# Performance work log

Measured on AMD Instinct MI355X. Metric: run time of the kernel, lower is better.

The kernel has to match this reference:

```python
import jax, jax.numpy as jnp
import numpy as np

N_HEADS = 8
D_EMBED = 512
D_HEAD = D_EMBED // N_HEADS


def setup_inputs() -> dict:
    key = jax.random.key(0)
    ks = jax.random.split(key, 5)
    B, S, D = 8, 2048, D_EMBED
    scale_in = 1.0 / np.sqrt(D)
    x = jax.random.normal(ks[0], (B, S, D), dtype=jnp.float32)
    # torch nn.Linear weights: (out_features, in_features)
    w_in = jax.random.normal(ks[1], (3 * D, D), dtype=jnp.float32) * scale_in
    b_in = jax.random.normal(ks[2], (3 * D,), dtype=jnp.float32) * scale_in
    w_out = jax.random.normal(ks[3], (D, D), dtype=jnp.float32) * scale_in
    b_out = jax.random.normal(ks[4], (D,), dtype=jnp.float32) * scale_in
    return {"x": x, "w_in": w_in, "b_in": b_in, "w_out": w_out, "b_out": b_out}


def reference(x, w_in, b_in, w_out, b_out):
    B, S, D = x.shape
    H, Dh = N_HEADS, D_HEAD
    # fused QKV projection (torch Linear: x @ W^T + b)
    qkv = x @ w_in.T + b_in                     # (B, S, 3D)
    q, k, v = jnp.split(qkv, 3, axis=-1)        # each (B, S, D)
    # split heads -> (B, H, S, Dh)
    def heads(t):
        return t.reshape(B, S, H, Dh).transpose(0, 2, 1, 3)
    q, k, v = heads(q), heads(k), heads(v)
    # scaled dot-product attention (full matrix, as in source)
    scores = jnp.einsum("bhqd,bhkd->bhqk", q, k) / jnp.sqrt(jnp.float32(Dh))
    weights = jax.nn.softmax(scores, axis=-1)   # (B, H, S, S)
    out = jnp.einsum("bhqk,bhkd->bhqd", weights, v)
    out = out.transpose(0, 2, 1, 3).reshape(B, S, D)
    return out @ w_out.T + b_out
```

## Files before the change

### kernel.cpp

```cpp
#include <hip/hip_runtime.h>
#include <stdint.h>

#define SEQ   2048
#define DEMB  512
#define NH    8
#define DH    64
#define BATCH 8
#define M_ROWS (BATCH * SEQ)
#define QKLD  1024
#define QSCALE 0.18033688011112042f

typedef __attribute__((ext_vector_type(8))) __bf16 bf16x8;
typedef __attribute__((ext_vector_type(4))) __bf16 bf16x4;
typedef __attribute__((ext_vector_type(4))) float  f32x4;
typedef __attribute__((ext_vector_type(8))) uint16_t u16x8;
typedef __attribute__((ext_vector_type(4))) uint32_t u32x4;

__device__ __forceinline__ void gll16(const __bf16* g, __bf16* l) {
    __builtin_amdgcn_global_load_lds(
        (__attribute__((address_space(1))) void*)(__bf16*)g,
        (__attribute__((address_space(3))) void*)l, 16, 0, 0);
}

__device__ __forceinline__ bf16x8 ld8(const __bf16* p) {
    return *(const bf16x8*)p;
}

__device__ __forceinline__ uint32_t pkpair(float a, float b) {
    const uint16_t lo = __builtin_bit_cast(uint16_t, (__bf16)a);
    const uint16_t hi = __builtin_bit_cast(uint16_t, (__bf16)b);
    return (uint32_t)lo | ((uint32_t)hi << 16);
}

__device__ __forceinline__ int sw(int row, int chunk) {
    return row * 64 + ((chunk ^ (row & 7)) << 3);
}

__device__ __forceinline__ void stage_gll_sw(const __bf16* g, int gld,
                                             __bf16* l, int wave, int lane) {
    const int lr = lane >> 3;
    const int scol = ((lane & 7) ^ lr) * 8;
    #pragma unroll
    for (int i = 0; i < 2; i++) {
        const int r0 = i * 32 + wave * 8;
        gll16(g + (size_t)(r0 + lr) * gld + scol, l + r0 * 64);
    }
}

__device__ __forceinline__ void stage_gll(const __bf16* src, __bf16* dst,
                                          int ld, int wave, int lane) {
    const int srow = lane >> 3, scol = ((lane & 7) ^ srow) * 8;
    #pragma unroll
    for (int i = 0; i < 4; i++) {
        const int r0 = (i * 4 + wave) * 8;
        gll16(src + (size_t)(r0 + srow) * ld + scol, dst + r0 * 64);
    }
}

#define NXQ (M_ROWS * DEMB / 4)
#define NWQ (3 * DEMB * DEMB / 4)
#define NOQ (DEMB * DEMB / 4)

__global__ __launch_bounds__(256)
void cvt_all(const float* __restrict__ x, const float* __restrict__ w_in,
             __bf16* __restrict__ xb, __bf16* __restrict__ wb) {
    const int i = blockIdx.x * 256 + threadIdx.x;
    const float4* src;
    bf16x4* dst;
    if (i < NXQ) { src = (const float4*)x + i;         dst = (bf16x4*)xb + i; }
    else if (i < NXQ + NWQ) {
        const int j = i - NXQ;
        src = (const float4*)w_in + j;  dst = (bf16x4*)wb + j;
    } else return;
    const float4 v = *src;
    bf16x4 b;
    b[0] = (__bf16)v.x; b[1] = (__bf16)v.y;
    b[2] = (__bf16)v.z; b[3] = (__bf16)v.w;
    *dst = b;
}

__global__ __launch_bounds__(256)
void cvt_wout(const float* __restrict__ w, __bf16* __restrict__ wb) {
    const int i = blockIdx.x * 256 + threadIdx.x;
    if (i < NOQ) {
        const float4 v = ((const float4*)w)[i];
        bf16x4 b;
        b[0] = (__bf16)v.x; b[1] = (__bf16)v.y;
        b[2] = (__bf16)v.z; b[3] = (__bf16)v.w;
        ((bf16x4*)wb)[i] = b;
    }
}

__global__ __launch_bounds__(256)
void gemm_qkv(const __bf16* __restrict__ A, const __bf16* __restrict__ W,
              const float* __restrict__ bias, __bf16* __restrict__ qk,
              __bf16* __restrict__ vt) {
    constexpr int K = DEMB;
    __shared__ __align__(16) __bf16 SM[128 * 128];
    __bf16* As = SM;
    __bf16* Bs = SM + 128 * 64;

    const int tid  = threadIdx.x;
    const int wave = tid >> 6, lane = tid & 63;
    const int quad = lane >> 4, l16 = lane & 15;
    const int m0 = blockIdx.x * 128, n0 = blockIdx.y * 128;
    const int wm = wave & 1, wn = wave >> 1;
    const bool qkblk = (n0 < QKLD);

    f32x4 acc[4][4] = {};

    for (int k0 = 0; k0 < K; k0 += 64) {
        __syncthreads();
        stage_gll(A + (size_t)m0 * K + k0, As, K, wave, lane);
        stage_gll(W + (size_t)n0 * K + k0, Bs, K, wave, lane);
        __syncthreads();
        #pragma unroll
        for (int ks = 0; ks < 2; ks++) {
            bf16x8 af[4], bf[4];
            #pragma unroll
            for (int t = 0; t < 4; t++) {
                af[t] = ld8(&As[sw(wm * 64 + t * 16 + l16, ks * 4 + quad)]);
                bf[t] = ld8(&Bs[sw(wn * 64 + t * 16 + l16, ks * 4 + quad)]);
            }
            if (qkblk) {
                #pragma unroll
                for (int j = 0; j < 4; j++)
                    #pragma unroll
                    for (int i = 0; i < 4; i++)
                        acc[j][i] = __builtin_amdgcn_mfma_f32_16x16x32_bf16(
                            bf[j], af[i], acc[j][i], 0, 0, 0);
            } else {
                #pragma unroll
                for (int i = 0; i < 4; i++)
                    #pragma unroll
                    for (int j = 0; j < 4; j++)
                        acc[i][j] = __builtin_amdgcn_mfma_f32_16x16x32_bf16(
                            af[i], bf[j], acc[i][j], 0, 0, 0);
            }
        }
    }

    __syncthreads();

    if (qkblk) {
        const float scl = (n0 < DEMB) ? QSCALE : 1.0f;
        #pragma unroll
        for (int j = 0; j < 4; j++) {
            const int nl = wn * 64 + j * 16 + quad * 4;
            const float4 bv4 = *(const float4*)&bias[n0 + nl];
            const int chunk = nl >> 3;
            #pragma unroll
            for (int i = 0; i < 4; i++) {
                const int ml = wm * 64 + i * 16 + l16;
                bf16x4 pk;
                pk[0] = (__bf16)((acc[j][i][0] + bv4.x) * scl);
                pk[1] = (__bf16)((acc[j][i][1] + bv4.y) * scl);
                pk[2] = (__bf16)((acc[j][i][2] + bv4.z) * scl);
                pk[3] = (__bf16)((acc[j][i][3] + bv4.w) * scl);
                const int phys = ((chunk & 7) ^ (ml & 7)) | (chunk & 8);
                *(bf16x4*)(&SM[ml * 128 + phys * 8 + (nl & 7)]) = pk;
            }
        }
        __syncthreads();
        const int g = tid >> 4, li = tid & 15;
        #pragma unroll
        for (int it = 0; it < 8; it++) {
            const int row = it * 16 + g;
            const int phys = ((li & 7) ^ (row & 7)) | (li & 8);
            bf16x8 v = ld8(&SM[row * 128 + phys * 8]);
            *(bf16x8*)(qk + (size_t)(m0 + row) * QKLD + n0 + li * 8) = v;
        }
    } else {
        const int hd0 = n0 - QKLD;
        const int bb = m0 >> 11, s0 = m0 & (SEQ - 1);
        #pragma unroll
        for (int j = 0; j < 4; j++) {
            const int n = n0 + wn * 64 + j * 16 + l16;
            const float bv = bias[n];
            const int hdl = wn * 64 + j * 16 + l16;
            #pragma unroll
            for (int i = 0; i < 4; i++) {
                const int sl = wm * 64 + i * 16 + quad * 4;
                bf16x4 pk;
                #pragma unroll
                for (int r = 0; r < 4; r++)
                    pk[r] = (__bf16)(acc[i][j][r] + bv);
                const int chunk = sl >> 3;
                const int phys = (((chunk & 7) ^ (hdl & 7)) | (chunk & 8));
                *(bf16x4*)(&SM[hdl * 128 + phys * 8 + (sl & 7)]) = pk;
            }
        }
        __syncthreads();
        const int g = tid >> 4, li = tid & 15;
        #pragma unroll
        for (int it = 0; it < 8; it++) {
            const int row = it * 16 + g;
            const int phys = (((li & 7) ^ (row & 7)) | (li & 8));
            bf16x8 v = ld8(&SM[row * 128 + phys * 8]);
            *(bf16x8*)(vt + ((size_t)(bb * DEMB + hd0 + row)) * SEQ + s0 + li * 8) = v;
        }
    }
}

__global__ __launch_bounds__(256, 4)
void attn_flash(const __bf16* __restrict__ qk, const __bf16* __restrict__ vt,
                __bf16* __restrict__ outp) {
    const int qt = blockIdx.x, h = blockIdx.y, b = blockIdx.z;
    const int tid  = threadIdx.x;
    const int wave = tid >> 6, lane = tid & 63;
    const int quad = lane >> 4, l16 = lane & 15;

    __shared__ __align__(16) __bf16 Ks[2][64 * 64];
    __shared__ __align__(16) __bf16 Vt[2][64 * 64];

    const size_t brow = (size_t)b * SEQ;
    const int q0 = qt * 128 + wave * 32;
    const __bf16* kbase = qk + brow * QKLD + DEMB + h * DH;
    const __bf16* vbase = vt + ((size_t)(b * DEMB + h * DH)) * SEQ;

    const u16x8 one16 = {0x3F80, 0x3F80, 0x3F80, 0x3F80,
                         0x3F80, 0x3F80, 0x3F80, 0x3F80};
    const bf16x8 ONES = __builtin_bit_cast(bf16x8, one16);

    bf16x8 qf[2][2];
    #pragma unroll
    for (int qb = 0; qb < 2; qb++) {
        const __bf16* qp = qk + (brow + q0 + qb * 16 + l16) * QKLD + h * DH + quad * 8;
        qf[qb][0] = ld8(qp);
        qf[qb][1] = ld8(qp + 32);
    }

    f32x4 o[2][4] = {};
    f32x4 osum[2] = {};
    uint32_t pk[2][4][2];
    bf16x8 pf[2][2];

    auto do_qkexp = [&](int tt) {
        const int bufq = tt & 1;
        #pragma unroll
        for (int kt = 0; kt < 4; kt++) {
            bf16x8 kf0 = ld8(&Ks[bufq][sw(kt * 16 + l16, quad)]);
            bf16x8 kf1 = ld8(&Ks[bufq][sw(kt * 16 + l16, 4 + quad)]);
            #pragma unroll
            for (int qb = 0; qb < 2; qb++) {
                f32x4 c = {};
                c = __builtin_amdgcn_mfma_f32_16x16x32_bf16(kf0, qf[qb][0], c, 0, 0, 0);
                c = __builtin_amdgcn_mfma_f32_16x16x32_bf16(kf1, qf[qb][1], c, 0, 0, 0);
                pk[qb][kt][0] = pkpair(__builtin_amdgcn_exp2f(c[0]),
                                       __builtin_amdgcn_exp2f(c[1]));
                pk[qb][kt][1] = pkpair(__builtin_amdgcn_exp2f(c[2]),
                                       __builtin_amdgcn_exp2f(c[3]));
            }
        }
    };

    auto do_permlane_osum = [&]() {
        #pragma unroll
        for (int qb = 0; qb < 2; qb++) {
            #pragma unroll
            for (int f = 0; f < 2; f++) {
                uint32_t a0 = pk[qb][2 * f][0], b0 = pk[qb][2 * f + 1][0];
                uint32_t a1 = pk[qb][2 * f][1], b1 = pk[qb][2 * f + 1][1];
                {
                    auto r = __builtin_amdgcn_permlane32_swap(a0, b0, false, false);
                    a0 = r[0]; b0 = r[1];
                }
                {
                    auto r = __builtin_amdgcn_permlane32_swap(a1, b1, false, false);
                    a1 = r[0]; b1 = r[1];
                }
                {
                    auto r = __builtin_amdgcn_permlane16_swap(a0, b0, false, false);
                    a0 = r[0]; b0 = r[1];
                }
                {
                    auto r = __builtin_amdgcn_permlane16_swap(a1, b1, false, false);
                    a1 = r[0]; b1 = r[1];
                }
                u32x4 d;
                d[0] = a0; d[1] = a1; d[2] = b0; d[3] = b1;
                pf[qb][f] = __builtin_bit_cast(bf16x8, d);
            }
            osum[qb] = __builtin_amdgcn_mfma_f32_16x16x32_bf16(pf[qb][0], ONES, osum[qb], 0, 0, 0);
            osum[qb] = __builtin_amdgcn_mfma_f32_16x16x32_bf16(pf[qb][1], ONES, osum[qb], 0, 0, 0);
        }
    };

    auto do_pv = [&](int tt) {
        const int bufv = tt & 1;
        #pragma unroll
        for (int db = 0; db < 4; db++) {
            bf16x8 vf0 = ld8(&Vt[bufv][sw(db * 16 + l16, quad)]);
            bf16x8 vf1 = ld8(&Vt[bufv][sw(db * 16 + l16, 4 + quad)]);
            #pragma unroll
            for (int qb = 0; qb < 2; qb++) {
                o[qb][db] = __builtin_amdgcn_mfma_f32_16x16x32_bf16(pf[qb][0], vf0, o[qb][db], 0, 0, 0);
                o[qb][db] = __builtin_amdgcn_mfma_f32_16x16x32_bf16(pf[qb][1], vf1, o[qb][db], 0, 0, 0);
            }
        }
    };

    constexpr int NT = SEQ / 64;

    stage_gll_sw(kbase,                      QKLD, Ks[0], wave, lane);
    stage_gll_sw(vbase,                      SEQ,  Vt[0], wave, lane);
    stage_gll_sw(kbase + (size_t)64 * QKLD,  QKLD, Ks[1], wave, lane);
    __syncthreads();
    do_qkexp(0);

    for (int t = 0; t < NT - 1; ++t) {
        __syncthreads();
        if (t + 2 < NT)
            stage_gll_sw(kbase + (size_t)(t + 2) * 64 * QKLD, QKLD, Ks[t & 1], wave, lane);
        stage_gll_sw(vbase + (t + 1) * 64, SEQ, Vt[(t + 1) & 1], wave, lane);

        do_permlane_osum();
        __builtin_amdgcn_s_setprio(1);
        do_pv(t);
        do_qkexp(t + 1);
        __builtin_amdgcn_s_setprio(0);
    }

    __syncthreads();
    do_permlane_osum();
    do_pv(NT - 1);

    #pragma unroll
    for (int qb = 0; qb < 2; qb++)
        #pragma unroll
        for (int r = 0; r < 4; r++) {
            const float linv = __builtin_amdgcn_rcpf(osum[qb][r]);
            const int q = q0 + qb * 16 + quad * 4 + r;
            #pragma unroll
            for (int db = 0; db < 4; db++)
                outp[(brow + q) * DEMB + h * DH + db * 16 + l16] =
                    (__bf16)(o[qb][db][r] * linv);
        }
}

__global__ __launch_bounds__(256)
void gemm_out(const __bf16* __restrict__ A, const __bf16* __restrict__ W,
              const float* __restrict__ bias, float* __restrict__ C,
              int N, int K) {
    __shared__ __align__(16) __bf16 SMO[2 * 128 * 64];
    __bf16* As = SMO;
    __bf16* Bs = SMO + 128 * 64;

    const int tid  = threadIdx.x;
    const int wave = tid >> 6, lane = tid & 63;
    const int quad = lane >> 4, l16 = lane & 15;
    const int m0 = blockIdx.x * 128, n0 = blockIdx.y * 128;
    const int wm = wave & 1, wn = wave >> 1;

    f32x4 acc[4][4] = {};

    for (int k0 = 0; k0 < K; k0 += 64) {
        __syncthreads();
        stage_gll(A + (size_t)m0 * K + k0, As, K, wave, lane);
        stage_gll(W + (size_t)n0 * K + k0, Bs, K, wave, lane);
        __syncthreads();
        #pragma unroll
        for (int ks = 0; ks < 2; ks++) {
            bf16x8 af[4], bf[4];
            #pragma unroll
            for (int t = 0; t < 4; t++) {
                af[t] = ld8(&As[sw(wm * 64 + t * 16 + l16, ks * 4 + quad)]);
                bf[t] = ld8(&Bs[sw(wn * 64 + t * 16 + l16, ks * 4 + quad)]);
            }
            #pragma unroll
            for (int j = 0; j < 4; j++)
                #pragma unroll
                for (int i = 0; i < 4; i++)
                    acc[j][i] = __builtin_amdgcn_mfma_f32_16x16x32_bf16(
                        bf[j], af[i], acc[j][i], 0, 0, 0);
        }
    }

    __syncthreads();
    float* SMf = (float*)SMO;

    #pragma unroll
    for (int p = 0; p < 2; p++) {
        if (p) __syncthreads();
        if (wm == p) {
            #pragma unroll
            for (int j = 0; j < 4; j++) {
                const int nl = wn * 64 + j * 16 + quad * 4;
                const float4 bv4 = *(const float4*)&bias[n0 + nl];
                const int chunkf = nl >> 2;
                #pragma unroll
                for (int i = 0; i < 4; i++) {
                    const int ml = i * 16 + l16;
                    const int physf = ((chunkf & 7) ^ (ml & 7)) | (chunkf & 24);
                    float4 v;
                    v.x = acc[j][i][0] + bv4.x;
                    v.y = acc[j][i][1] + bv4.y;
                    v.z = acc[j][i][2] + bv4.z;
                    v.w = acc[j][i][3] + bv4.w;
                    *(float4*)(&SMf[ml * 128 + physf * 4]) = v;
                }
            }
        }
        __syncthreads();
        const int g2 = tid >> 5, li2 = tid & 31;
        #pragma unroll
        for (int it = 0; it < 8; it++) {
            const int row = it * 8 + g2;
            const int physf = ((li2 & 7) ^ (row & 7)) | (li2 & 24);
            float4 v = *(const float4*)&SMf[row * 128 + physf * 4];
            *(float4*)(&C[(size_t)(m0 + p * 64 + row) * N + n0 + li2 * 4]) = v;
        }
    }
}

extern "C" void kernel_launch(void* const* d_in, const int* in_sizes, int n_in,
                              void* d_out, int out_size, void* d_ws, size_t ws_size,
                              hipStream_t stream) {
    const float* x     = (const float*)d_in[0];
    const float* w_in  = (const float*)d_in[1];
    const float* b_in  = (const float*)d_in[2];
    const float* w_out = (const float*)d_in[3];
    const float* b_out = (const float*)d_in[4];

    __bf16* qk   = (__bf16*)d_ws;
    __bf16* vtb  = qk + (size_t)M_ROWS * QKLD;
    __bf16* xbuf = vtb + (size_t)BATCH * DEMB * SEQ;
    __bf16* aout = xbuf;
    __bf16* woutb = vtb;
    __bf16* winb = (__bf16*)((char*)d_out + 24u * 1024 * 1024);
    float*  outp = (float*)d_out;

    cvt_all<<<(NXQ + NWQ + 255) / 256, 256, 0, stream>>>(x, w_in, xbuf, winb);
    gemm_qkv<<<dim3(M_ROWS / 128, 12), 256, 0, stream>>>(xbuf, winb, b_in, qk, vtb);
    attn_flash<<<dim3(SEQ / 128, NH, BATCH), 256, 0, stream>>>(qk, vtb, aout);
    cvt_wout<<<NOQ / 256, 256, 0, stream>>>(w_out, woutb);
    gemm_out<<<dim3(M_ROWS / 128, DEMB / 128), 256, 0, stream>>>(
        aout, woutb, b_out, outp, DEMB, DEMB);
}
```

Baseline: 227.4 us.

## Double-buffer K=32 LDS tiles in QKV and output projection GEMMs

Both projection GEMMs now stage 32-wide K slices into two LDS buffers, using a new 32-column swizzle. The next slice's global-to-LDS loads are issued right after a single barrier, so they overlap with the MFMA work on the current slice. This replaces the old pattern of two barriers per 64-wide K step with a serialized load then compute. The cost is more loop iterations, each with less MFMA work per barrier. It also depends on the barrier draining the asynchronous LDS loads.

New measurement: 224.2 us (median of 2 runs). Within noise of the previous version (-1.4%).

```diff
diff --git a/kernel.cpp b/kernel.cpp
--- a/kernel.cpp
+++ b/kernel.cpp
@@ -36,6 +36,10 @@
     return row * 64 + ((chunk ^ (row & 7)) << 3);
 }
 
+__device__ __forceinline__ int sw32(int row, int chunk) {
+    return row * 32 + ((chunk ^ ((row >> 1) & 3)) << 3);
+}
+
 __device__ __forceinline__ void stage_gll_sw(const __bf16* g, int gld,
                                              __bf16* l, int wave, int lane) {
     const int lr = lane >> 3;
@@ -47,13 +51,14 @@
     }
 }
 
-__device__ __forceinline__ void stage_gll(const __bf16* src, __bf16* dst,
-                                          int ld, int wave, int lane) {
-    const int srow = lane >> 3, scol = ((lane & 7) ^ srow) * 8;
+__device__ __forceinline__ void stage_gll32(const __bf16* src, __bf16* dst,
+                                            int ld, int wave, int lane) {
+    const int lr = lane >> 2;
+    const int scol = ((lane & 3) ^ ((lr >> 1) & 3)) * 8;
     #pragma unroll
-    for (int i = 0; i < 4; i++) {
-        const int r0 = (i * 4 + wave) * 8;
-        gll16(src + (size_t)(r0 + srow) * ld + scol, dst + r0 * 64);
+    for (int i = 0; i < 2; i++) {
+        const int r0 = (i * 4 + wave) * 16;
+        gll16(src + (size_t)(r0 + lr) * ld + scol, dst + r0 * 32);
     }
 }
 
@@ -97,8 +102,6 @@
               __bf16* __restrict__ vt) {
     constexpr int K = DEMB;
     __shared__ __align__(16) __bf16 SM[128 * 128];
-    __bf16* As = SM;
-    __bf16* Bs = SM + 128 * 64;
 
     const int tid  = threadIdx.x;
     const int wave = tid >> 6, lane = tid & 63;
@@ -109,34 +112,40 @@
 
     f32x4 acc[4][4] = {};
 
-    for (int k0 = 0; k0 < K; k0 += 64) {
-        __syncthreads();
-        stage_gll(A + (size_t)m0 * K + k0, As, K, wave, lane);
-        stage_gll(W + (size_t)n0 * K + k0, Bs, K, wave, lane);
-        __syncthreads();
-        #pragma unroll
-        for (int ks = 0; ks < 2; ks++) {
-            bf16x8 af[4], bf[4];
-            #pragma unroll
-            for (int t = 0; t < 4; t++) {
-                af[t] = ld8(&As[sw(wm * 64 + t * 16 + l16, ks * 4 + quad)]);
-                bf[t] = ld8(&Bs[sw(wn * 64 + t * 16 + l16, ks * 4 + quad)]);
-            }
-            if (qkblk) {
+    const __bf16* Ab = A + (size_t)m0 * K;
+    const __bf16* Wb = W + (size_t)n0 * K;
+
+    stage_gll32(Ab, SM, K, wave, lane);
+    stage_gll32(Wb, SM + 8192, K, wave, lane);
+
+    for (int t = 0; t < K / 32; ++t) {
+        __syncthreads();
+        if (t + 1 < K / 32) {
+            const int nb = (t + 1) & 1;
+            stage_gll32(Ab + (t + 1) * 32, SM + nb * 4096, K, wave, lane);
+            stage_gll32(Wb + (t + 1) * 32, SM + 8192 + nb * 4096, K, wave, lane);
+        }
+        const int buf = t & 1;
+        bf16x8 af[4], bf[4];
+        #pragma unroll
+        for (int tt = 0; tt < 4; tt++) {
+            af[tt] = ld8(&SM[buf * 4096 + sw32(wm * 64 + tt * 16 + l16, quad)]);
+            bf[tt] = ld8(&SM[8192 + buf * 4096 + sw32(wn * 64 + tt * 16 + l16, quad)]);
+        }
+        if (qkblk) {
+            #pragma unroll
+            for (int j = 0; j < 4; j++)
+                #pragma unroll
+                for (int i = 0; i < 4; i++)
+                    acc[j][i] = __builtin_amdgcn_mfma_f32_16x16x32_bf16(
+                        bf[j], af[i], acc[j][i], 0, 0, 0);
+        } else {
+            #pragma unroll
+            for (int i = 0; i < 4; i++)
                 #pragma unroll
                 for (int j = 0; j < 4; j++)
-                    #pragma unroll
-                    for (int i = 0; i < 4; i++)
-                        acc[j][i] = __builtin_amdgcn_mfma_f32_16x16x32_bf16(
-                            bf[j], af[i], acc[j][i], 0, 0, 0);
-            } else {
-                #pragma unroll
-                for (int i = 0; i < 4; i++)
-                    #pragma unroll
-                    for (int j = 0; j < 4; j++)
-                        acc[i][j] = __builtin_amdgcn_mfma_f32_16x16x32_bf16(
-                            af[i], bf[j], acc[i][j], 0, 0, 0);
-            }
+                    acc[i][j] = __builtin_amdgcn_mfma_f32_16x16x32_bf16(
+                        af[i], bf[j], acc[i][j], 0, 0, 0);
         }
     }
 
@@ -342,9 +351,7 @@
 void gemm_out(const __bf16* __restrict__ A, const __bf16* __restrict__ W,
               const float* __restrict__ bias, float* __restrict__ C,
               int N, int K) {
-    __shared__ __align__(16) __bf16 SMO[2 * 128 * 64];
-    __bf16* As = SMO;
-    __bf16* Bs = SMO + 128 * 64;
+    __shared__ __align__(16) __bf16 SMO[128 * 128];
 
     const int tid  = threadIdx.x;
     const int wave = tid >> 6, lane = tid & 63;
@@ -354,26 +361,32 @@
 
     f32x4 acc[4][4] = {};
 
-    for (int k0 = 0; k0 < K; k0 += 64) {
-        __syncthreads();
-        stage_gll(A + (size_t)m0 * K + k0, As, K, wave, lane);
-        stage_gll(W + (size_t)n0 * K + k0, Bs, K, wave, lane);
-        __syncthreads();
-        #pragma unroll
-        for (int ks = 0; ks < 2; ks++) {
-            bf16x8 af[4], bf[4];
-            #pragma unroll
-            for (int t = 0; t < 4; t++) {
-                af[t] = ld8(&As[sw(wm * 64 + t * 16 + l16, ks * 4 + quad)]);
-                bf[t] = ld8(&Bs[sw(wn * 64 + t * 16 + l16, ks * 4 + quad)]);
-            }
-            #pragma unroll
-            for (int j = 0; j < 4; j++)
-                #pragma unroll
-                for (int i = 0; i < 4; i++)
-                    acc[j][i] = __builtin_amdgcn_mfma_f32_16x16x32_bf16(
-                        bf[j], af[i], acc[j][i], 0, 0, 0);
-        }
+    const __bf16* Ab = A + (size_t)m0 * K;
+    const __bf16* Wb = W + (size_t)n0 * K;
+
+    stage_gll32(Ab, SMO, K, wave, lane);
+    stage_gll32(Wb, SMO + 8192, K, wave, lane);
+
+    for (int t = 0; t < K / 32; ++t) {
+        __syncthreads();
+        if (t + 1 < K / 32) {
+            const int nb = (t + 1) & 1;
+            stage_gll32(Ab + (t + 1) * 32, SMO + nb * 4096, K, wave, lane);
+            stage_gll32(Wb + (t + 1) * 32, SMO + 8192 + nb * 4096, K, wave, lane);
+        }
+        const int buf = t & 1;
+        bf16x8 af[4], bf[4];
+        #pragma unroll
+        for (int tt = 0; tt < 4; tt++) {
+            af[tt] = ld8(&SMO[buf * 4096 + sw32(wm * 64 + tt * 16 + l16, quad)]);
+            bf[tt] = ld8(&SMO[8192 + buf * 4096 + sw32(wn * 64 + tt * 16 + l16, quad)]);
+        }
+        #pragma unroll
+        for (int j = 0; j < 4; j++)
+            #pragma unroll
+            for (int i = 0; i < 4; i++)
+                acc[j][i] = __builtin_amdgcn_mfma_f32_16x16x32_bf16(
+                    bf[j], af[i], acc[j][i], 0, 0, 0);
     }
 
     __syncthreads();
```
